# Kernel tuning notes

Hardware: AMD Instinct MI355X
Metric: run time of the kernel (lower is better)

## Reference

```python
import jax, jax.numpy as jnp
import numpy as np

T, B, I, H = 1024, 64, 512, 512


def setup_inputs() -> dict:
    key = jax.random.key(0)
    ks = jax.random.split(key, 7)
    s_in = 1.0 / np.sqrt(H)
    return {
        "input": jax.random.normal(ks[0], (T, B, I), jnp.float32),
        "h0": jax.random.normal(ks[1], (B, H), jnp.float32),
        "c0": jax.random.normal(ks[2], (B, H), jnp.float32),
        "W_ih": jax.random.normal(ks[3], (4 * H, I), jnp.float32) * s_in,
        "W_hh": jax.random.normal(ks[4], (4 * H, H), jnp.float32) * s_in,
        "b_ih": jax.random.normal(ks[5], (4 * H,), jnp.float32) * s_in,
        "b_hh": jax.random.normal(ks[6], (4 * H,), jnp.float32) * s_in,
    }


def reference(input, h0, c0, W_ih, W_hh, b_ih, b_hh):
    # Precompute input projections for all timesteps in one big GEMM: [T,B,4H]
    x_proj = jnp.einsum('tbi,gi->tbg', input, W_ih) + b_ih + b_hh

    def step(carry, x_p):
        h, c = carry
        gates = jax.nn.sigmoid(x_p + h @ W_hh.T)  # [B,4H], all gates sigmoid (subLSTM)
        i, f, z, o = jnp.split(gates, 4, axis=-1)
        c_new = f * c + z - i
        h_new = jax.nn.sigmoid(c_new) - o
        return (h_new, c_new), h_new

    # reverse=True == torch code: reverse inputs, scan, reverse outputs back
    (h_f, c_f), outputs = jax.lax.scan(step, (h0, c0), x_proj, reverse=True)
    return outputs, (h_f, c_f)
```

## Files before the change

### kernel.cpp

```cpp
#include <hip/hip_runtime.h>
#include <hip/hip_bf16.h>

typedef float  f32x2  __attribute__((ext_vector_type(2)));
typedef float  f32x4  __attribute__((ext_vector_type(4)));
typedef float  f32x16 __attribute__((ext_vector_type(16)));
typedef __bf16 bfrag8 __attribute__((ext_vector_type(8)));
typedef __bf16 bf16x4 __attribute__((ext_vector_type(4)));

#define T_STEPS 1024
#define BB 64
#define II 512
#define HH 512
#define G4 2048
#define NB 64
#define BH (BB*HH)

static __device__ inline unsigned short bf16_bits(float f) {
  union { __bf16 h; unsigned short u; } v; v.h = (__bf16)f; return v.u;
}

__global__ void k_init_h(const float* __restrict__ h0, unsigned* __restrict__ hb) {
  int i = blockIdx.x * 256 + threadIdx.x;
  hb[i] = ((unsigned)bf16_bits(h0[i]) << 16);
}

template<bool XF32>
__global__ __launch_bounds__(256) void k_xproj(
    const float* __restrict__ inp, const float* __restrict__ Wih,
    const float* __restrict__ bih, const float* __restrict__ bhh,
    void* __restrict__ xp_) {
  constexpr int BM = 128, BN = 128, BK = 64, LDK = 72;
  __shared__ __bf16 As[BM][LDK];
  __shared__ __bf16 Bs[BN][LDK];
  const int bx = blockIdx.x;
  const int tm = bx >> 4, tn = bx & 15;
  const int m0 = tm * BM, n0 = tn * BN;
  const int tid = threadIdx.x;
  const int lane = tid & 63, w = tid >> 6;
  const int wm = w >> 1, wn = w & 1;
  const int l31 = lane & 31, lhi = lane >> 5;

  f32x16 acc[2][2] = {};

  const int srow = tid >> 2;
  const int sq = tid & 3;

  for (int k0 = 0; k0 < 512; k0 += BK) {
    __syncthreads();
    #pragma unroll
    for (int j = 0; j < 2; j++) {
      const int r = srow + 64 * j;
      const float* pa = inp + (size_t)(m0 + r) * II + k0 + sq * 16;
      const float* pb = Wih + (size_t)(n0 + r) * II + k0 + sq * 16;
      #pragma unroll
      for (int i = 0; i < 4; i++) {
        f32x4 va = *(const f32x4*)(pa + 4 * i);
        bf16x4 wa; wa[0]=(__bf16)va[0]; wa[1]=(__bf16)va[1]; wa[2]=(__bf16)va[2]; wa[3]=(__bf16)va[3];
        *(bf16x4*)&As[r][sq * 16 + 4 * i] = wa;
        f32x4 vb = *(const f32x4*)(pb + 4 * i);
        bf16x4 wb; wb[0]=(__bf16)vb[0]; wb[1]=(__bf16)vb[1]; wb[2]=(__bf16)vb[2]; wb[3]=(__bf16)vb[3];
        *(bf16x4*)&Bs[r][sq * 16 + 4 * i] = wb;
      }
    }
    __syncthreads();
    #pragma unroll
    for (int ks = 0; ks < 4; ks++) {
      const int kk = ks * 16 + 8 * lhi;
      bfrag8 af0 = *(const bfrag8*)&As[64 * wm +      l31][kk];
      bfrag8 af1 = *(const bfrag8*)&As[64 * wm + 32 + l31][kk];
      bfrag8 bf0 = *(const bfrag8*)&Bs[64 * wn +      l31][kk];
      bfrag8 bf1 = *(const bfrag8*)&Bs[64 * wn + 32 + l31][kk];
      acc[0][0] = __builtin_amdgcn_mfma_f32_32x32x16_bf16(af0, bf0, acc[0][0], 0, 0, 0);
      acc[0][1] = __builtin_amdgcn_mfma_f32_32x32x16_bf16(af0, bf1, acc[0][1], 0, 0, 0);
      acc[1][0] = __builtin_amdgcn_mfma_f32_32x32x16_bf16(af1, bf0, acc[1][0], 0, 0, 0);
      acc[1][1] = __builtin_amdgcn_mfma_f32_32x32x16_bf16(af1, bf1, acc[1][1], 0, 0, 0);
    }
  }
  #pragma unroll
  for (int a = 0; a < 2; a++)
    #pragma unroll
    for (int b = 0; b < 2; b++) {
      const int col = n0 + 64 * wn + 32 * b + l31;
      const float bias = bih[col] + bhh[col];
      #pragma unroll
      for (int q = 0; q < 16; q++) {
        const int row = m0 + 64 * wm + 32 * a + (q & 3) + 8 * (q >> 2) + 4 * lhi;
        const float v = acc[a][b][q] + bias;
        if constexpr (XF32) ((float*)xp_)[(size_t)row * G4 + col] = v;
        else                ((__bf16*)xp_)[(size_t)row * G4 + col] = (__bf16)v;
      }
    }
}

template<bool XF32>
__global__ __launch_bounds__(256, 1) void k_recur(
    const float* __restrict__ Whh, const float* __restrict__ c0,
    const void* __restrict__ xp_, unsigned* __restrict__ hb,
    float* __restrict__ out) {
  const int bid = blockIdx.x;
  const int rb = bid & 1;
  const int g  = bid >> 1;
  const int tid = threadIdx.x;
  const int lane = tid & 63, w = tid >> 6;
  const int tt = w & 1, kh = w >> 1;
  const int l31 = lane & 31, lhi = lane >> 5;

  __shared__ __bf16 hA[32][520];
  __shared__ float pRed[2][32][32];
  __shared__ float gLds[4][32][16];

  const int gate = tt * 2 + (l31 >> 4);
  const int gcol = gate * 512 + g * 16 + (l31 & 15);

  bfrag8 bw[16];
  #pragma unroll
  for (int ks = 0; ks < 16; ks++) {
    const float* p = Whh + (size_t)gcol * HH + kh * 256 + ks * 16 + 8 * lhi;
    f32x4 v0 = *(const f32x4*)p;
    f32x4 v1 = *(const f32x4*)(p + 4);
    bfrag8 f;
    f[0]=(__bf16)v0[0]; f[1]=(__bf16)v0[1]; f[2]=(__bf16)v0[2]; f[3]=(__bf16)v0[3];
    f[4]=(__bf16)v1[0]; f[5]=(__bf16)v1[1]; f[6]=(__bf16)v1[2]; f[7]=(__bf16)v1[3];
    bw[ks] = f;
  }

  const int lb = tid >> 3, c2 = (tid & 7) * 2;
  const int brow = 32 * rb + lb;
  const int jcol = 16 * g + c2;
  f32x2 creg = *(const f32x2*)(c0 + (size_t)brow * HH + jcol);

  const int str = w * 8 + (lane >> 3);
  const int sb  = lane & 7;

  for (int s = 0; s < T_STEPS; s++) {
    const int t = T_STEPS - 1 - s;

    f32x16 xv = {};
    if (kh == 0) {
      #pragma unroll
      for (int q = 0; q < 16; q++) {
        const int row = (q & 3) + 8 * (q >> 2) + 4 * lhi;
        const size_t idx = ((size_t)t * BB + 32 * rb + row) * G4 + gcol;
        if constexpr (XF32) xv[q] = ((const float*)xp_)[idx];
        else                xv[q] = (float)((const __bf16*)xp_)[idx];
      }
    }

    const unsigned long long* hrow = (const unsigned long long*)
        (hb + (size_t)(s & 1) * BH + (size_t)(32 * rb + str) * HH);
    const unsigned long long tpat = 0x0000FFFF0000FFFFull;
    const unsigned long long texp = (unsigned long long)s * 0x0000000100000001ull;
    unsigned long long v[32];
    for (;;) {
      int ok = 1;
      #pragma unroll
      for (int i = 0; i < 32; i++)
        v[i] = __hip_atomic_load(hrow + sb + 8 * i,
                                 __ATOMIC_RELAXED, __HIP_MEMORY_SCOPE_AGENT);
      #pragma unroll
      for (int i = 0; i < 32; i++) ok &= ((v[i] & tpat) == texp);
      if (ok) break;
    }
    #pragma unroll
    for (int i = 0; i < 32; i++) {
      const unsigned lo = (unsigned)v[i], hi = (unsigned)(v[i] >> 32);
      const unsigned packed = (lo >> 16) | (hi & 0xFFFF0000u);
      *(unsigned*)&hA[str][(sb + 8 * i) * 2] = packed;
    }
    __syncthreads();

    f32x16 acc = {};
    #pragma unroll
    for (int ks = 0; ks < 16; ks++) {
      bfrag8 a = *(const bfrag8*)&hA[l31][kh * 256 + ks * 16 + 8 * lhi];
      acc = __builtin_amdgcn_mfma_f32_32x32x16_bf16(a, bw[ks], acc, 0, 0, 0);
    }
    if (kh == 1) {
      #pragma unroll
      for (int q = 0; q < 16; q++) {
        const int row = (q & 3) + 8 * (q >> 2) + 4 * lhi;
        pRed[tt][row][l31] = acc[q];
      }
    }
    __syncthreads();
    if (kh == 0) {
      #pragma unroll
      for (int q = 0; q < 16; q++) {
        const int row = (q & 3) + 8 * (q >> 2) + 4 * lhi;
        const float vv = acc[q] + pRed[tt][row][l31] + xv[q];
        gLds[gate][row][l31 & 15] = 1.f / (1.f + __expf(-vv));
      }
    }
    __syncthreads();

    {
      const float i0 = gLds[0][lb][c2],     i1 = gLds[0][lb][c2 + 1];
      const float f0 = gLds[1][lb][c2],     f1 = gLds[1][lb][c2 + 1];
      const float z0 = gLds[2][lb][c2],     z1 = gLds[2][lb][c2 + 1];
      const float o0 = gLds[3][lb][c2],     o1 = gLds[3][lb][c2 + 1];
      const float cn0 = f0 * creg[0] + z0 - i0;
      const float cn1 = f1 * creg[1] + z1 - i1;
      creg[0] = cn0; creg[1] = cn1;
      const float hn0 = 1.f / (1.f + __expf(-cn0)) - o0;
      const float hn1 = 1.f / (1.f + __expf(-cn1)) - o1;
      const unsigned tag = (unsigned)(s + 1);
      const unsigned plo = ((unsigned)bf16_bits(hn0) << 16) | tag;
      const unsigned phi = ((unsigned)bf16_bits(hn1) << 16) | tag;
      const unsigned long long pv = ((unsigned long long)phi << 32) | plo;
      __hip_atomic_store((unsigned long long*)
          (hb + (size_t)((s + 1) & 1) * BH + (size_t)brow * HH + jcol),
          pv, __ATOMIC_RELAXED, __HIP_MEMORY_SCOPE_AGENT);
      f32x2 hv; hv[0] = hn0; hv[1] = hn1;
      __builtin_nontemporal_store(hv,
          (f32x2*)(out + (size_t)t * BH + (size_t)brow * HH + jcol));
      if (s == T_STEPS - 1) {
        f32x2 cv; cv[0] = cn0; cv[1] = cn1;
        *(f32x2*)(out + (size_t)T_STEPS * BH + (size_t)brow * HH + jcol) = hv;
        *(f32x2*)(out + (size_t)T_STEPS * BH + BH + (size_t)brow * HH + jcol) = cv;
      }
    }
  }
}

extern "C" void kernel_launch(void* const* d_in, const int* in_sizes, int n_in,
                              void* d_out, int out_size, void* d_ws, size_t ws_size,
                              hipStream_t stream) {
  (void)in_sizes; (void)n_in; (void)out_size;
  const float* inp = (const float*)d_in[0];
  const float* h0  = (const float*)d_in[1];
  const float* c0  = (const float*)d_in[2];
  const float* Wih = (const float*)d_in[3];
  const float* Whh = (const float*)d_in[4];
  const float* bih = (const float*)d_in[5];
  const float* bhh = (const float*)d_in[6];
  float* out = (float*)d_out;
  char* ws = (char*)d_ws;

  unsigned* hb = (unsigned*)ws;
  void*     xp = (void*)(ws + (1u << 20));
  const size_t need_f32 = (1u << 20) + (size_t)T_STEPS * BB * G4 * 4;
  const bool xf32 = ws_size >= need_f32;

  k_init_h<<<BH / 256, 256, 0, stream>>>(h0, hb);
  const int gemm_grid = (T_STEPS * BB / 128) * (G4 / 128);
  if (xf32) {
    k_xproj<true ><<<gemm_grid, 256, 0, stream>>>(inp, Wih, bih, bhh, xp);
    k_recur<true ><<<NB, 256, 0, stream>>>(Whh, c0, xp, hb, out);
  } else {
    k_xproj<false><<<gemm_grid, 256, 0, stream>>>(inp, Wih, bih, bhh, xp);
    k_recur<false><<<NB, 256, 0, stream>>>(Whh, c0, xp, hb, out);
  }
}
```

Measured before the change: 5.245 ms.

## Cut per-step barriers, prefetch next x-projection, and re-poll only stale h words

```diff
diff --git a/kernel.cpp b/kernel.cpp
--- a/kernel.cpp
+++ b/kernel.cpp
@@ -18,10 +18,12 @@
 static __device__ inline unsigned short bf16_bits(float f) {
   union { __bf16 h; unsigned short u; } v; v.h = (__bf16)f; return v.u;
 }
+static __device__ inline float sigm(float x) { return 1.f / (1.f + __expf(-x)); }
 
 __global__ void k_init_h(const float* __restrict__ h0, unsigned* __restrict__ hb) {
   int i = blockIdx.x * 256 + threadIdx.x;
-  hb[i] = ((unsigned)bf16_bits(h0[i]) << 16);
+  if (i < BH) hb[i] = ((unsigned)bf16_bits(h0[i]) << 16);
+  else        hb[i] = 0x0000FFFFu;
 }
 
 template<bool XF32>
@@ -106,8 +108,7 @@
   const int l31 = lane & 31, lhi = lane >> 5;
 
   __shared__ __bf16 hA[32][520];
-  __shared__ float pRed[2][32][32];
-  __shared__ float gLds[4][32][16];
+  __shared__ float pS[2][2][32][33];
 
   const int gate = tt * 2 + (l31 >> 4);
   const int gcol = gate * 512 + g * 16 + (l31 & 15);
@@ -132,34 +133,41 @@
   const int str = w * 8 + (lane >> 3);
   const int sb  = lane & 7;
 
+  int xrow[16];
+  #pragma unroll
+  for (int q = 0; q < 16; q++) xrow[q] = (q & 3) + 8 * (q >> 2) + 4 * lhi;
+
+  f32x16 xv_cur = {}, xv_nxt = {};
+  if (kh == 0) {
+    #pragma unroll
+    for (int q = 0; q < 16; q++) {
+      const size_t idx = ((size_t)(T_STEPS - 1) * BB + 32 * rb + xrow[q]) * G4 + gcol;
+      if constexpr (XF32) xv_cur[q] = ((const float*)xp_)[idx];
+      else                xv_cur[q] = (float)((const __bf16*)xp_)[idx];
+    }
+  }
+
   for (int s = 0; s < T_STEPS; s++) {
     const int t = T_STEPS - 1 - s;
-
-    f32x16 xv = {};
-    if (kh == 0) {
-      #pragma unroll
-      for (int q = 0; q < 16; q++) {
-        const int row = (q & 3) + 8 * (q >> 2) + 4 * lhi;
-        const size_t idx = ((size_t)t * BB + 32 * rb + row) * G4 + gcol;
-        if constexpr (XF32) xv[q] = ((const float*)xp_)[idx];
-        else                xv[q] = (float)((const __bf16*)xp_)[idx];
-      }
-    }
 
     const unsigned long long* hrow = (const unsigned long long*)
         (hb + (size_t)(s & 1) * BH + (size_t)(32 * rb + str) * HH);
     const unsigned long long tpat = 0x0000FFFF0000FFFFull;
     const unsigned long long texp = (unsigned long long)s * 0x0000000100000001ull;
     unsigned long long v[32];
+    unsigned need = 0xFFFFFFFFu;
     for (;;) {
-      int ok = 1;
       #pragma unroll
       for (int i = 0; i < 32; i++)
-        v[i] = __hip_atomic_load(hrow + sb + 8 * i,
-                                 __ATOMIC_RELAXED, __HIP_MEMORY_SCOPE_AGENT);
-      #pragma unroll
-      for (int i = 0; i < 32; i++) ok &= ((v[i] & tpat) == texp);
-      if (ok) break;
+        if (need & (1u << i))
+          v[i] = __hip_atomic_load(hrow + sb + 8 * i,
+                                   __ATOMIC_RELAXED, __HIP_MEMORY_SCOPE_AGENT);
+      unsigned miss = 0;
+      #pragma unroll
+      for (int i = 0; i < 32; i++)
+        if ((need & (1u << i)) && ((v[i] & tpat) != texp)) miss |= 1u << i;
+      if (miss == 0) break;
+      need = miss;
     }
     #pragma unroll
     for (int i = 0; i < 32; i++) {
@@ -167,6 +175,15 @@
       const unsigned packed = (lo >> 16) | (hi & 0xFFFF0000u);
       *(unsigned*)&hA[str][(sb + 8 * i) * 2] = packed;
     }
+
+    if (kh == 0 && s + 1 < T_STEPS) {
+      #pragma unroll
+      for (int q = 0; q < 16; q++) {
+        const size_t idx = ((size_t)(t - 1) * BB + 32 * rb + xrow[q]) * G4 + gcol;
+        if constexpr (XF32) xv_nxt[q] = ((const float*)xp_)[idx];
+        else                xv_nxt[q] = (float)((const __bf16*)xp_)[idx];
+      }
+    }
     __syncthreads();
 
     f32x16 acc = {};
@@ -175,34 +192,29 @@
       bfrag8 a = *(const bfrag8*)&hA[l31][kh * 256 + ks * 16 + 8 * lhi];
       acc = __builtin_amdgcn_mfma_f32_32x32x16_bf16(a, bw[ks], acc, 0, 0, 0);
     }
-    if (kh == 1) {
-      #pragma unroll
-      for (int q = 0; q < 16; q++) {
-        const int row = (q & 3) + 8 * (q >> 2) + 4 * lhi;
-        pRed[tt][row][l31] = acc[q];
-      }
-    }
-    __syncthreads();
-    if (kh == 0) {
-      #pragma unroll
-      for (int q = 0; q < 16; q++) {
-        const int row = (q & 3) + 8 * (q >> 2) + 4 * lhi;
-        const float vv = acc[q] + pRed[tt][row][l31] + xv[q];
-        gLds[gate][row][l31 & 15] = 1.f / (1.f + __expf(-vv));
-      }
+    #pragma unroll
+    for (int q = 0; q < 16; q++) {
+      const int row = (q & 3) + 8 * (q >> 2) + 4 * lhi;
+      pS[kh][tt][row][l31] = (kh == 0) ? (acc[q] + xv_cur[q]) : acc[q];
     }
     __syncthreads();
 
     {
-      const float i0 = gLds[0][lb][c2],     i1 = gLds[0][lb][c2 + 1];
-      const float f0 = gLds[1][lb][c2],     f1 = gLds[1][lb][c2 + 1];
-      const float z0 = gLds[2][lb][c2],     z1 = gLds[2][lb][c2 + 1];
-      const float o0 = gLds[3][lb][c2],     o1 = gLds[3][lb][c2 + 1];
-      const float cn0 = f0 * creg[0] + z0 - i0;
-      const float cn1 = f1 * creg[1] + z1 - i1;
+      float sg[4][2];
+      #pragma unroll
+      for (int gt = 0; gt < 4; gt++) {
+        const int tl = gt >> 1, off = (gt & 1) * 16;
+        #pragma unroll
+        for (int dc = 0; dc < 2; dc++) {
+          const int col = off + c2 + dc;
+          sg[gt][dc] = sigm(pS[0][tl][lb][col] + pS[1][tl][lb][col]);
+        }
+      }
+      const float cn0 = sg[1][0] * creg[0] + sg[2][0] - sg[0][0];
+      const float cn1 = sg[1][1] * creg[1] + sg[2][1] - sg[0][1];
       creg[0] = cn0; creg[1] = cn1;
-      const float hn0 = 1.f / (1.f + __expf(-cn0)) - o0;
-      const float hn1 = 1.f / (1.f + __expf(-cn1)) - o1;
+      const float hn0 = sigm(cn0) - sg[3][0];
+      const float hn1 = sigm(cn1) - sg[3][1];
       const unsigned tag = (unsigned)(s + 1);
       const unsigned plo = ((unsigned)bf16_bits(hn0) << 16) | tag;
       const unsigned phi = ((unsigned)bf16_bits(hn1) << 16) | tag;
@@ -219,6 +231,7 @@
         *(f32x2*)(out + (size_t)T_STEPS * BH + BH + (size_t)brow * HH + jcol) = cv;
       }
     }
+    xv_cur = xv_nxt;
   }
 }
 
@@ -241,7 +254,7 @@
   const size_t need_f32 = (1u << 20) + (size_t)T_STEPS * BB * G4 * 4;
   const bool xf32 = ws_size >= need_f32;
 
-  k_init_h<<<BH / 256, 256, 0, stream>>>(h0, hb);
+  k_init_h<<<2 * BH / 256, 256, 0, stream>>>(h0, hb);
   const int gemm_grid = (T_STEPS * BB / 128) * (G4 / 128);
   if (xf32) {
     k_xproj<true ><<<gemm_grid, 256, 0, stream>>>(inp, Wih, bih, bhh, xp);
```

Result: slower. 5.400 ms (+3.0%).
